# Optimization experiments

Hardware: AMD Instinct MI355X
Metric: run time of the kernel (lower is better)

## Reference

```python
import jax, jax.numpy as jnp
import numpy as np

# Model dims
L, B, S, D, H, V = 8, 4, 1024, 1024, 16, 256
FF = 4 * D
LN_EPS = 1e-5


def _ln(x, g, b):
    mu = jnp.mean(x, axis=-1, keepdims=True)
    var = jnp.mean(jnp.square(x - mu), axis=-1, keepdims=True)
    return (x - mu) * jax.lax.rsqrt(var + LN_EPS) * g + b


def setup_inputs() -> dict:
    key = jax.random.key(0)
    ks = jax.random.split(key, 12)
    p = lambda k, shape: (jax.random.normal(k, shape, jnp.float32) * 0.02)
    return {
        "input_tokens": jax.random.randint(ks[0], (B, S), 0, V),
        "tok_emb": p(ks[1], (V, D)),
        "pos_emb": p(ks[2], (S, D)),
        "Wq": p(ks[3], (L, D, D)),
        "Wk": p(ks[4], (L, D, D)),
        "Wv": p(ks[5], (L, D, D)),
        "Wo": p(ks[6], (L, D, D)),
        "bo": jnp.zeros((L, D), jnp.float32),
        "ln1_g": jnp.ones((L, D), jnp.float32),
        "ln1_b": jnp.zeros((L, D), jnp.float32),
        "ln2_g": jnp.ones((L, D), jnp.float32),
        "ln2_b": jnp.zeros((L, D), jnp.float32),
        "W1": p(ks[7], (L, D, FF)),
        "b1": jnp.zeros((L, FF), jnp.float32),
        "W2": p(ks[8], (L, FF, D)),
        "b2": jnp.zeros((L, D), jnp.float32),
        "lnf_g": jnp.ones((D,), jnp.float32),
        "lnf_b": jnp.zeros((D,), jnp.float32),
        "Wout": p(ks[9], (D, V)),
        "bout": jnp.zeros((V,), jnp.float32),
        "nhead": 16,
    }


def reference(input_tokens, tok_emb, pos_emb, Wq, Wk, Wv, Wo, bo,
              ln1_g, ln1_b, ln2_g, ln2_b, W1, b1, W2, b2,
              lnf_g, lnf_b, Wout, bout, nhead):
    b, s = input_tokens.shape
    d = tok_emb.shape[-1]
    hd = d // nhead
    scale = jnp.asarray(hd, jnp.float32) ** -0.5  # head_size ** -0.5
    mask = jnp.tril(jnp.ones((s, s), bool))  # causal

    x = tok_emb[input_tokens] + pos_emb[:s][None]  # [b,s,d]

    def block(x, p):
        wq, wk, wv, wo, bo_, g1, be1, g2, be2, w1, bf1, w2, bf2 = p
        h = _ln(x, g1, be1)
        q = (h @ wq).reshape(b, s, nhead, hd)
        k = (h @ wk).reshape(b, s, nhead, hd)
        v = (h @ wv).reshape(b, s, nhead, hd)
        scores = jnp.einsum('bqhd,bkhd->bhqk', q, k) * scale
        scores = jnp.where(mask, scores, -jnp.inf)
        attn = jax.nn.softmax(scores, axis=-1)  # dropout is identity (p=0 / eval)
        o = jnp.einsum('bhqk,bkhd->bqhd', attn, v).reshape(b, s, d)
        x = x + o @ wo + bo_
        h2 = _ln(x, g2, be2)
        x = x + jax.nn.relu(h2 @ w1 + bf1) @ w2 + bf2
        return x, None

    x, _ = jax.lax.scan(block, x, (Wq, Wk, Wv, Wo, bo, ln1_g, ln1_b,
                                   ln2_g, ln2_b, W1, b1, W2, b2))
    logits = _ln(x, lnf_g, lnf_b) @ Wout + bout  # [b,s,V]
    return logits
```

## Files before the change

kernel.cpp:

```cpp
#include <hip/hip_runtime.h>

#define DEV __device__ __forceinline__

typedef __bf16 bf16x8 __attribute__((ext_vector_type(8)));
typedef float  f32x4  __attribute__((ext_vector_type(4)));

typedef const __attribute__((address_space(1))) unsigned int* gas_ptr;
typedef       __attribute__((address_space(3))) unsigned int* las_ptr;

DEV unsigned short f2bf(float f) {
  union { __bf16 h; unsigned short u; } c; c.h = (__bf16)f; return c.u;
}

DEV float bf2f(unsigned short u) {
  union { unsigned int i; float f; } c; c.i = (unsigned int)u << 16; return c.f;
}

DEV void gll16(const void* g, void* l) {
  __builtin_amdgcn_global_load_lds((gas_ptr)g, (las_ptr)l, 16, 0, 0);
}

DEV f32x4 mfma16(bf16x8 a, bf16x8 b, f32x4 c) {
  return __builtin_amdgcn_mfma_f32_16x16x32_bf16(a, b, c, 0, 0, 0);
}

__global__ __launch_bounds__(256)
void tcvt_k(const float* __restrict__ src, unsigned short* __restrict__ dst,
            int K, int N)
{
  __shared__ float t[32][33];
  const int tx = threadIdx.x, ty = threadIdx.y;
  const size_t mo = (size_t)blockIdx.z * K * N;
  const int n0 = blockIdx.x * 32, k0 = blockIdx.y * 32;
  const float* s = src + mo;
  unsigned short* d = dst + mo;
#pragma unroll
  for (int i = 0; i < 4; i++)
    t[ty + i*8][tx] = s[(size_t)(k0 + ty + i*8) * N + n0 + tx];
  __syncthreads();
#pragma unroll
  for (int i = 0; i < 4; i++)
    d[(size_t)(n0 + ty + i*8) * K + k0 + tx] = f2bf(t[tx][ty + i*8]);
}

DEV void ln_tail(float4 s, const float* __restrict__ g,
                 const float* __restrict__ bta,
                 unsigned short* __restrict__ hrow, int t, float* red)
{
  float sm  = s.x + s.y + s.z + s.w;
  float sq = s.x*s.x + s.y*s.y + s.z*s.z + s.w*s.w;
#pragma unroll
  for (int mk = 32; mk >= 1; mk >>= 1) {
    sm += __shfl_xor(sm, mk);
    sq += __shfl_xor(sq, mk);
  }
  const int wv = t >> 6;
  if ((t & 63) == 0) { red[wv] = sm; red[4 + wv] = sq; }
  __syncthreads();
  sm = red[0] + red[1] + red[2] + red[3];
  sq = red[4] + red[5] + red[6] + red[7];
  const float mu = sm * (1.f/1024.f);
  const float rs = rsqrtf(sq * (1.f/1024.f) - mu*mu + 1e-5f);
  const float4 gv = ((const float4*)g)[t];
  const float4 bv = ((const float4*)bta)[t];
  ushort4 o;
  o.x = f2bf((s.x - mu) * rs * gv.x + bv.x);
  o.y = f2bf((s.y - mu) * rs * gv.y + bv.y);
  o.z = f2bf((s.z - mu) * rs * gv.z + bv.z);
  o.w = f2bf((s.w - mu) * rs * gv.w + bv.w);
  ((ushort4*)hrow)[t] = o;
}

__global__ __launch_bounds__(256)
void embed_ln_k(const int* __restrict__ toks, const float* __restrict__ te,
                const float* __restrict__ pe, const float* __restrict__ g,
                const float* __restrict__ bta,
                float* __restrict__ x, unsigned short* __restrict__ h)
{
  __shared__ float red[8];
  const int row = blockIdx.x, t = threadIdx.x;
  const int tok = toks[row], s = row & 1023;
  float4 a = ((const float4*)(te + (size_t)tok * 1024))[t];
  float4 p = ((const float4*)(pe + (size_t)s   * 1024))[t];
  float4 v; v.x = a.x+p.x; v.y = a.y+p.y; v.z = a.z+p.z; v.w = a.w+p.w;
  ((float4*)(x + (size_t)row * 1024))[t] = v;
  ln_tail(v, g, bta, h + (size_t)row * 1024, t, red);
}

__global__ __launch_bounds__(256)
void redln_k(const unsigned short* __restrict__ part,
             const float* __restrict__ bias,
             const float* __restrict__ g, const float* __restrict__ bta,
             float* __restrict__ x, unsigned short* __restrict__ h)
{
  __shared__ float red[8];
  const int row = blockIdx.x, t = threadIdx.x;
  const size_t pbase = (size_t)row * 1024 + t * 4;
  float a0 = 0.f, a1 = 0.f, a2 = 0.f, a3 = 0.f;
#pragma unroll
  for (int kz = 0; kz < 4; kz++) {
    ushort4 u = *(const ushort4*)&part[(size_t)kz * 4194304 + pbase];
    a0 += bf2f(u.x); a1 += bf2f(u.y); a2 += bf2f(u.z); a3 += bf2f(u.w);
  }
  float4 xv = ((const float4*)(x + (size_t)row * 1024))[t];
  float4 bv = ((const float4*)bias)[t];
  float4 s;
  s.x = xv.x + a0 + bv.x; s.y = xv.y + a1 + bv.y;
  s.z = xv.z + a2 + bv.z; s.w = xv.w + a3 + bv.w;
  ((float4*)(x + (size_t)row * 1024))[t] = s;
  ln_tail(s, g, bta, h + (size_t)row * 1024, t, red);
}

template<int EPI>
__global__ __launch_bounds__(256)
void gemm_k(const unsigned short* __restrict__ A,
            const unsigned short* __restrict__ B0,
            const unsigned short* __restrict__ B1,
            const unsigned short* __restrict__ B2,
            const float* __restrict__ bias,
            float* __restrict__ xio,
            unsigned short* __restrict__ o0,
            unsigned short* __restrict__ o1,
            unsigned short* __restrict__ o2,
            int K, int N, int Kc, float* __restrict__ part)
{
  __shared__ __align__(16) unsigned short As[2][128 * 32];
  __shared__ __align__(16) unsigned short Bs[2][128 * 32];
  const int tid = threadIdx.x;
  const int wave = tid >> 6, lane = tid & 63;
  const int wm = wave >> 1, wn = wave & 1;
  const int m0 = blockIdx.x * 128, n0 = blockIdx.y * 128;
  const int r16 = lane & 15, r4 = lane >> 4;

  const unsigned short* Bt = B0;
  if (EPI == 0) Bt = (blockIdx.z == 0) ? B0 : (blockIdx.z == 1) ? B1 : B2;
  const int koff = (EPI >= 4) ? blockIdx.z * Kc : 0;
  const int klen = (EPI >= 4) ? Kc : K;

  const unsigned short* ga = A  + (size_t)(m0 + (tid >> 2)) * K + koff + (tid & 3) * 8;
  const unsigned short* gb = Bt + (size_t)(n0 + (tid >> 2)) * K + koff + (tid & 3) * 8;
  const size_t rstep = (size_t)64 * K;
  const int lo = wave * 512;

  auto STAGE = [&](int slot, int tt) {
    const unsigned short* gaa = ga + tt * 32;
    const unsigned short* gbb = gb + tt * 32;
    gll16(gaa,         &As[slot][lo]);
    gll16(gaa + rstep, &As[slot][lo + 2048]);
    gll16(gbb,         &Bs[slot][lo]);
    gll16(gbb + rstep, &Bs[slot][lo + 2048]);
  };

  f32x4 acc[4][4] = {};
  const int NT = klen >> 5;

  STAGE(0, 0);
  if (NT > 1) STAGE(1, 1);

  for (int t = 0; t < NT; t++) {
    if (t + 1 < NT) asm volatile("s_waitcnt vmcnt(4)" ::: "memory");
    else            asm volatile("s_waitcnt vmcnt(0)" ::: "memory");
    __builtin_amdgcn_sched_barrier(0);
    __builtin_amdgcn_s_barrier();
    __builtin_amdgcn_sched_barrier(0);

    const int slot = t & 1;
    bf16x8 av[4], bv[4];
#pragma unroll
    for (int mf = 0; mf < 4; mf++)
      av[mf] = *(const bf16x8*)&As[slot][(wm*64 + mf*16 + r16) * 32 + r4 * 8];
#pragma unroll
    for (int nf = 0; nf < 4; nf++)
      bv[nf] = *(const bf16x8*)&Bs[slot][(wn*64 + nf*16 + r16) * 32 + r4 * 8];
    asm volatile("s_waitcnt lgkmcnt(0)" ::: "memory");
    __builtin_amdgcn_sched_barrier(0);
    __builtin_amdgcn_s_barrier();
    __builtin_amdgcn_sched_barrier(0);

    if (t + 2 < NT) STAGE(slot, t + 2);

#pragma unroll
    for (int mf = 0; mf < 4; mf++)
#pragma unroll
      for (int nf = 0; nf < 4; nf++)
        acc[mf][nf] = mfma16(av[mf], bv[nf], acc[mf][nf]);
    __builtin_amdgcn_sched_barrier(0);
  }

  const int row0 = m0 + wm * 64, col0 = n0 + wn * 64;
  float* po = nullptr;
  if (EPI == 4)
    po = part + (size_t)blockIdx.z * ((size_t)gridDim.x * 128 * N);
  unsigned short* po16 = nullptr;
  if (EPI == 5)
    po16 = o0 + (size_t)blockIdx.z * 4194304;
#pragma unroll
  for (int mf = 0; mf < 4; mf++) {
#pragma unroll
    for (int nf = 0; nf < 4; nf++) {
#pragma unroll
      for (int jj = 0; jj < 4; jj++) {
        const int r = row0 + mf*16 + r4*4 + jj;
        const int c = col0 + nf*16 + r16;
        const float v = acc[mf][nf][jj];
        if (EPI == 0) {
          const int z = blockIdx.z;
          const int b_ = r >> 10, s_ = r & 1023;
          const int hh = c >> 6, e = c & 63;
          if (z == 0)
            o0[((size_t)(b_*16 + hh) * 1024 + s_) * 64 + e] = f2bf(v * 0.125f);
          else if (z == 1)
            o1[((size_t)(b_*16 + hh) * 1024 + s_) * 64 + e] = f2bf(v);
          else
            o2[((size_t)(b_*16 + hh) * 64 + e) * 1024 + s_] = f2bf(v);
        } else if (EPI == 2) {
          const float t2 = v + bias[c];
          o0[(size_t)r * N + c] = f2bf(t2 > 0.f ? t2 : 0.f);
        } else if (EPI == 4) {
          po[(size_t)r * N + c] = v;
        } else if (EPI == 5) {
          po16[(size_t)r * N + c] = f2bf(v);
        }
      }
    }
  }
}

template<int EPI>
__global__ __launch_bounds__(512, 2)
void gemm8_k(const unsigned short* __restrict__ A,
             const unsigned short* __restrict__ Bt,
             const float* __restrict__ bias,
             unsigned short* __restrict__ o0,
             int K, int N, int Kc)
{
  __shared__ __align__(16) unsigned short LA[2][2][8192];
  __shared__ __align__(16) unsigned short LB[2][2][8192];
  const int tid = threadIdx.x;
  const int wave = tid >> 6, lane = tid & 63;
  const int wm = wave >> 2, wn = wave & 3;
  const int r16 = lane & 15, r4 = lane >> 4;
  const int m0 = blockIdx.x * 256, n0 = blockIdx.y * 256;
  const int koff = blockIdx.z * Kc;
  const int NT = Kc >> 6;

  const unsigned short* As0 = A  + (size_t)m0 * K + koff;
  const unsigned short* As1 = A  + (size_t)(m0 + 128) * K + koff;
  const unsigned short* Bs0 = Bt + (size_t)n0 * K + koff;
  const unsigned short* Bs1 = Bt + (size_t)(n0 + 128) * K + koff;

  auto STAGEH = [&](unsigned short* lds, const unsigned short* gsrc) {
    const int c0 = tid, r0 = c0 >> 3;
    gll16(gsrc + (size_t)r0 * K + ((c0 & 7) ^ (r0 & 7)) * 8, lds + c0 * 8);
    const int c1 = 512 + tid, r1 = c1 >> 3;
    gll16(gsrc + (size_t)r1 * K + ((c1 & 7) ^ (r1 & 7)) * 8, lds + c1 * 8);
  };

  f32x4 acc[8][4] = {};
  bf16x8 avx[4][2], bvx[2][2][2];

  STAGEH(&LB[0][0][0], Bs0);
  STAGEH(&LB[0][1][0], Bs1);
  STAGEH(&LA[0][0][0], As0);
  STAGEH(&LA[0][1][0], As1);
  if (NT > 1) {
    STAGEH(&LB[1][0][0], Bs0 + 64);
    STAGEH(&LB[1][1][0], Bs1 + 64);
  }

  for (int t = 0; t < NT; ++t) {
    const int slot = t & 1;
    if (t + 1 < NT) asm volatile("s_waitcnt vmcnt(4)" ::: "memory");
    else            asm volatile("s_waitcnt vmcnt(0)" ::: "memory");
    __builtin_amdgcn_sched_barrier(0);
    __builtin_amdgcn_s_barrier();
    __builtin_amdgcn_sched_barrier(0);

#pragma unroll
    for (int mfq = 0; mfq < 4; mfq++)
#pragma unroll
      for (int kk = 0; kk < 2; kk++)
        avx[mfq][kk] = *(const bf16x8*)&LA[slot][wm][
            (mfq*16 + r16) * 64 + (((kk*4 + r4) ^ (r16 & 7)) * 8)];
#pragma unroll
    for (int nfq = 0; nfq < 2; nfq++)
#pragma unroll
      for (int kk = 0; kk < 2; kk++)
        bvx[0][nfq][kk] = *(const bf16x8*)&LB[slot][wn >> 1][
            ((wn & 1)*64 + nfq*16 + r16) * 64 + (((kk*4 + r4) ^ (r16 & 7)) * 8)];
    if (t + 1 < NT) STAGEH(&LA[slot ^ 1][0][0], As0 + (t + 1) * 64);
    asm volatile("s_waitcnt lgkmcnt(0)" ::: "memory");
    __builtin_amdgcn_sched_barrier(0);
    __builtin_amdgcn_s_setprio(1);
#pragma unroll
    for (int mfq = 0; mfq < 4; mfq++)
#pragma unroll
      for (int nfq = 0; nfq < 2; nfq++)
#pragma unroll
        for (int kk = 0; kk < 2; kk++)
          acc[mfq][nfq] = mfma16(avx[mfq][kk], bvx[0][nfq][kk], acc[mfq][nfq]);
    __builtin_amdgcn_s_setprio(0);

#pragma unroll
    for (int nfq = 0; nfq < 2; nfq++)
#pragma unroll
      for (int kk = 0; kk < 2; kk++)
        bvx[1][nfq][kk] = *(const bf16x8*)&LB[slot][wn >> 1][
            ((wn & 1)*64 + 32 + nfq*16 + r16) * 64 + (((kk*4 + r4) ^ (r16 & 7)) * 8)];
    if (t + 1 < NT) STAGEH(&LA[slot ^ 1][1][0], As1 + (t + 1) * 64);
    asm volatile("s_waitcnt lgkmcnt(0)" ::: "memory");
    __builtin_amdgcn_sched_barrier(0);
    __builtin_amdgcn_s_setprio(1);
#pragma unroll
    for (int mfq = 0; mfq < 4; mfq++)
#pragma unroll
      for (int nfq = 0; nfq < 2; nfq++)
#pragma unroll
        for (int kk = 0; kk < 2; kk++)
          acc[mfq][2 + nfq] = mfma16(avx[mfq][kk], bvx[1][nfq][kk], acc[mfq][2 + nfq]);
    __builtin_amdgcn_s_setprio(0);

    __builtin_amdgcn_sched_barrier(0);
    __builtin_amdgcn_s_barrier();
    __builtin_amdgcn_sched_barrier(0);

#pragma unroll
    for (int mfq = 0; mfq < 4; mfq++)
#pragma unroll
      for (int kk = 0; kk < 2; kk++)
        avx[mfq][kk] = *(const bf16x8*)&LA[slot][wm][
            (64 + mfq*16 + r16) * 64 + (((kk*4 + r4) ^ (r16 & 7)) * 8)];
    if (t + 2 < NT) STAGEH(&LB[slot][0][0], Bs0 + (t + 2) * 64);
    asm volatile("s_waitcnt lgkmcnt(0)" ::: "memory");
    __builtin_amdgcn_sched_barrier(0);
    __builtin_amdgcn_s_setprio(1);
#pragma unroll
    for (int mfq = 0; mfq < 4; mfq++)
#pragma unroll
      for (int nfq = 0; nfq < 2; nfq++)
#pragma unroll
        for (int kk = 0; kk < 2; kk++)
          acc[4 + mfq][nfq] = mfma16(avx[mfq][kk], bvx[0][nfq][kk], acc[4 + mfq][nfq]);
    __builtin_amdgcn_s_setprio(0);

    if (t + 2 < NT) STAGEH(&LB[slot][1][0], Bs1 + (t + 2) * 64);
    __builtin_amdgcn_s_setprio(1);
#pragma unroll
    for (int mfq = 0; mfq < 4; mfq++)
#pragma unroll
      for (int nfq = 0; nfq < 2; nfq++)
#pragma unroll
        for (int kk = 0; kk < 2; kk++)
          acc[4 + mfq][2 + nfq] = mfma16(avx[mfq][kk], bvx[1][nfq][kk], acc[4 + mfq][2 + nfq]);
    __builtin_amdgcn_s_setprio(0);
    __builtin_amdgcn_sched_barrier(0);
  }

  const int row0 = m0 + wm * 128, col0 = n0 + wn * 64;
  unsigned short* po16 = o0;
  if (EPI == 5) po16 = o0 + (size_t)blockIdx.z * 4194304;
#pragma unroll
  for (int mf = 0; mf < 8; mf++) {
#pragma unroll
    for (int nf = 0; nf < 4; nf++) {
#pragma unroll
      for (int jj = 0; jj < 4; jj++) {
        const int r = row0 + mf*16 + r4*4 + jj;
        const int c = col0 + nf*16 + r16;
        const float v = acc[mf][nf][jj];
        if (EPI == 2) {
          const float t2 = v + bias[c];
          po16[(size_t)r * N + c] = f2bf(t2 > 0.f ? t2 : 0.f);
        } else {
          po16[(size_t)r * N + c] = f2bf(v);
        }
      }
    }
  }
}

__global__ __launch_bounds__(256)
void red_k(const float* __restrict__ part, const float* __restrict__ bias,
           float* __restrict__ outw, int n4, int nm4, int KZ)
{
  const float4* p4 = (const float4*)part;
  const float4* b4 = (const float4*)bias;
  for (size_t i = (size_t)blockIdx.x * 256 + threadIdx.x; i < (size_t)n4;
       i += (size_t)gridDim.x * 256) {
    float4 s = p4[i];
    for (int kz = 1; kz < KZ; kz++) {
      float4 t = p4[i + (size_t)kz * n4];
      s.x += t.x; s.y += t.y; s.z += t.z; s.w += t.w;
    }
    float4 bv = b4[i & nm4];
    s.x += bv.x; s.y += bv.y; s.z += bv.z; s.w += bv.w;
    ((float4*)outw)[i] = s;
  }
}

__global__ __launch_bounds__(256)
void attn_k(const unsigned short* __restrict__ qb,
            const unsigned short* __restrict__ kb,
            const unsigned short* __restrict__ vtb,
            unsigned short* __restrict__ att)
{
  __shared__ __align__(16) unsigned short Ks[2][64 * 64];
  __shared__ __align__(16) unsigned short Vs[2][64 * 64];
  __shared__ __align__(16) unsigned short Ps[64 * 72];
  const int flat = blockIdx.x;
  const int job  = (flat & 7) * 128 + (flat >> 3);
  const int qt   = 15 - (job & 15);
  const int h    = (job >> 4) & 15;
  const int b    = job >> 8;
  const int tid = threadIdx.x, wave = tid >> 6, lane = tid & 63;
  const int r16 = lane & 15, r4 = lane >> 4;
  const int q0 = qt * 64;
  const size_t bh = (size_t)(b * 16 + h);
  const unsigned short* qbh = qb  + bh * 1024 * 64;
  const unsigned short* kbh = kb  + bh * 1024 * 64;
  const unsigned short* vbh = vtb + bh * 64 * 1024;

  const int swz = ((lane & 7) ^ (lane >> 3)) * 8;
  const int srow = lane >> 3;

  auto STAGE = [&](int slot, int tt) {
    const int kv0 = tt * 64;
#pragma unroll
    for (int cc = 0; cc < 2; cc++) {
      const int chunk = wave * 2 + cc;
      gll16(kbh + (size_t)(kv0 + chunk*8 + srow) * 64 + swz,   &Ks[slot][chunk * 512]);
      gll16(vbh + (size_t)(chunk*8 + srow) * 1024 + kv0 + swz, &Vs[slot][chunk * 512]);
    }
  };

  bf16x8 qf[2];
#pragma unroll
  for (int kc = 0; kc < 2; kc++)
    qf[kc] = *(const bf16x8*)&qbh[(size_t)(q0 + wave*16 + r16) * 64 + kc*32 + r4*8];

  f32x4 oacc[4] = {};
  float l_i[4] = {0.f, 0.f, 0.f, 0.f};

  const int nt = qt + 1;

  STAGE(0, 0);
  if (nt > 1) STAGE(1, 1);

  for (int t = 0; t < nt; t++) {
    if (t + 1 < nt) asm volatile("s_waitcnt vmcnt(4)" ::: "memory");
    else            asm volatile("s_waitcnt vmcnt(0)" ::: "memory");
    __builtin_amdgcn_sched_barrier(0);
    __builtin_amdgcn_s_barrier();
    __builtin_amdgcn_sched_barrier(0);

    const int slot = t & 1;
    bf16x8 kf[2][4], vf[2][4];
#pragma unroll
    for (int kc = 0; kc < 2; kc++)
#pragma unroll
      for (int nf = 0; nf < 4; nf++) {
        kf[kc][nf] = *(const bf16x8*)&Ks[slot][(nf*16 + r16) * 64 +
                                              (((kc*4 + r4) ^ (r16 & 7)) * 8)];
        vf[kc][nf] = *(const bf16x8*)&Vs[slot][(nf*16 + r16) * 64 +
                                              (((kc*4 + r4) ^ (r16 & 7)) * 8)];
      }
    asm volatile("s_waitcnt lgkmcnt(0)" ::: "memory");
    __builtin_amdgcn_sched_barrier(0);
    __builtin_amdgcn_s_barrier();
    __builtin_amdgcn_sched_barrier(0);

    if (t + 2 < nt) STAGE(slot, t + 2);

    f32x4 sacc[4] = {};
#pragma unroll
    for (int kc = 0; kc < 2; kc++)
#pragma unroll
      for (int nf = 0; nf < 4; nf++)
        sacc[nf] = mfma16(qf[kc], kf[kc][nf], sacc[nf]);

    const bool diag = (t == nt - 1);
#pragma unroll
    for (int jj = 0; jj < 4; jj++) {
      float vv[4];
#pragma unroll
      for (int nf = 0; nf < 4; nf++) vv[nf] = sacc[nf][jj];
      if (diag) {
        const int qrow_l = wave*16 + r4*4 + jj;
#pragma unroll
        for (int nf = 0; nf < 4; nf++)
          if (nf*16 + r16 > qrow_l) vv[nf] = -1e30f;
      }
      float p0 = __expf(vv[0]), p1 = __expf(vv[1]);
      float p2 = __expf(vv[2]), p3 = __expf(vv[3]);
      l_i[jj] += (p0 + p1) + (p2 + p3);
      const int prow = (wave*16 + r4*4 + jj) * 72;
      Ps[prow + r16     ] = f2bf(p0);
      Ps[prow + 16 + r16] = f2bf(p1);
      Ps[prow + 32 + r16] = f2bf(p2);
      Ps[prow + 48 + r16] = f2bf(p3);
    }

#pragma unroll
    for (int kc = 0; kc < 2; kc++) {
      bf16x8 pf = *(const bf16x8*)&Ps[(wave*16 + r16) * 72 + kc*32 + r4*8];
#pragma unroll
      for (int nh = 0; nh < 4; nh++)
        oacc[nh] = mfma16(pf, vf[kc][nh], oacc[nh]);
    }
    __builtin_amdgcn_sched_barrier(0);
  }

#pragma unroll
  for (int jj = 0; jj < 4; jj++)
#pragma unroll
    for (int mk = 8; mk >= 1; mk >>= 1) l_i[jj] += __shfl_xor(l_i[jj], mk);

#pragma unroll
  for (int nh = 0; nh < 4; nh++) {
#pragma unroll
    for (int jj = 0; jj < 4; jj++) {
      const int row = q0 + wave*16 + r4*4 + jj;
      const int col = nh*16 + r16;
      const float o = oacc[nh][jj] / l_i[jj];
      att[(size_t)(b * 1024 + row) * 1024 + h*64 + col] = f2bf(o);
    }
  }
}

extern "C" void kernel_launch(void* const* d_in, const int* in_sizes, int n_in,
                              void* d_out, int out_size, void* d_ws, size_t ws_size,
                              hipStream_t stream)
{
  const int*   toks    = (const int*)  d_in[0];
  const float* tok_emb = (const float*)d_in[1];
  const float* pos_emb = (const float*)d_in[2];
  const float* Wq      = (const float*)d_in[3];
  const float* Wk      = (const float*)d_in[4];
  const float* Wv      = (const float*)d_in[5];
  const float* Wo      = (const float*)d_in[6];
  const float* bo      = (const float*)d_in[7];
  const float* ln1_g   = (const float*)d_in[8];
  const float* ln1_b   = (const float*)d_in[9];
  const float* ln2_g   = (const float*)d_in[10];
  const float* ln2_b   = (const float*)d_in[11];
  const float* W1      = (const float*)d_in[12];
  const float* b1      = (const float*)d_in[13];
  const float* W2      = (const float*)d_in[14];
  const float* b2      = (const float*)d_in[15];
  const float* lnf_g   = (const float*)d_in[16];
  const float* lnf_b   = (const float*)d_in[17];
  const float* Wout    = (const float*)d_in[18];
  const float* bout    = (const float*)d_in[19];
  float* out = (float*)d_out;

  char* w = (char*)d_ws;
  size_t off = 0;
  auto alloc = [&](size_t bytes) -> void* {
    void* p = w + off; off += (bytes + 255) & ~(size_t)255; return p;
  };
  unsigned short* wqT   = (unsigned short*)alloc(8ull*1024*1024*2);
  unsigned short* wkT   = (unsigned short*)alloc(8ull*1024*1024*2);
  unsigned short* wvT   = (unsigned short*)alloc(8ull*1024*1024*2);
  unsigned short* woT   = (unsigned short*)alloc(8ull*1024*1024*2);
  unsigned short* w1T   = (unsigned short*)alloc(8ull*1024*4096*2);
  unsigned short* w2T   = (unsigned short*)alloc(8ull*4096*1024*2);
  unsigned short* woutT = (unsigned short*)alloc(256ull*1024*2);
  float*          x     = (float*)         alloc(4096ull*1024*4);
  unsigned short* hbuf  = (unsigned short*)alloc(4096ull*1024*2);
  unsigned short* qbuf  = (unsigned short*)alloc(64ull*1024*64*2);
  unsigned short* kbuf  = (unsigned short*)alloc(64ull*1024*64*2);
  unsigned short* vtb   = (unsigned short*)alloc(64ull*1024*64*2);
  unsigned short* att   = (unsigned short*)alloc(4096ull*1024*2);
  unsigned short* ff    = (unsigned short*)alloc(4096ull*4096*2);
  unsigned short* part16= (unsigned short*)alloc(4ull*4194304*2);
  float*          part  = (float*)         alloc(8ull*1048576*4);
  (void)ws_size; (void)in_sizes; (void)n_in; (void)out_size;

  dim3 tb(32, 8);
  tcvt_k<<<dim3(32, 32, 8),  tb, 0, stream>>>(Wq,   wqT,   1024, 1024);
  tcvt_k<<<dim3(32, 32, 8),  tb, 0, stream>>>(Wk,   wkT,   1024, 1024);
  tcvt_k<<<dim3(32, 32, 8),  tb, 0, stream>>>(Wv,   wvT,   1024, 1024);
  tcvt_k<<<dim3(32, 32, 8),  tb, 0, stream>>>(Wo,   woT,   1024, 1024);
  tcvt_k<<<dim3(128, 32, 8), tb, 0, stream>>>(W1,   w1T,   1024, 4096);
  tcvt_k<<<dim3(32, 128, 8), tb, 0, stream>>>(W2,   w2T,   4096, 1024);
  tcvt_k<<<dim3(8, 32, 1),   tb, 0, stream>>>(Wout, woutT, 1024, 256);

  embed_ln_k<<<4096, 256, 0, stream>>>(toks, tok_emb, pos_emb,
                                       ln1_g, ln1_b, x, hbuf);

  for (int l = 0; l < 8; l++) {
    gemm_k<0><<<dim3(32, 8, 3), 256, 0, stream>>>(hbuf,
        wqT + (size_t)l*1048576, wkT + (size_t)l*1048576, wvT + (size_t)l*1048576,
        nullptr, nullptr, qbuf, kbuf, vtb, 1024, 1024, 1024, nullptr);
    attn_k<<<1024, 256, 0, stream>>>(qbuf, kbuf, vtb, att);
    gemm_k<5><<<dim3(32, 8, 4), 256, 0, stream>>>(att,
        woT + (size_t)l*1048576, nullptr, nullptr,
        nullptr, nullptr, part16, nullptr, nullptr, 1024, 1024, 256, nullptr);
    redln_k<<<4096, 256, 0, stream>>>(part16, bo + l*1024,
        ln2_g + l*1024, ln2_b + l*1024, x, hbuf);
    gemm8_k<2><<<dim3(16, 16), 512, 0, stream>>>(hbuf,
        w1T + (size_t)l*4194304, b1 + l*4096, ff, 1024, 4096, 1024);
    gemm8_k<5><<<dim3(16, 4, 4), 512, 0, stream>>>(ff,
        w2T + (size_t)l*4194304, nullptr, part16, 4096, 1024, 1024);
    if (l < 7)
      redln_k<<<4096, 256, 0, stream>>>(part16, b2 + l*1024,
          ln1_g + (l+1)*1024, ln1_b + (l+1)*1024, x, hbuf);
    else
      redln_k<<<4096, 256, 0, stream>>>(part16, b2 + l*1024,
          lnf_g, lnf_b, x, hbuf);
  }

  gemm_k<4><<<dim3(32, 2, 8), 256, 0, stream>>>(hbuf, woutT, nullptr, nullptr,
      nullptr, nullptr, nullptr, nullptr, nullptr, 1024, 256, 128, part);
  red_k<<<1024, 256, 0, stream>>>(part, bout, out, 262144, 63, 8);
}
```

Measured before the change: 1.707 ms.

## Move QKV and out-proj GEMMs to 256x256 tile kernel; enlarge attention q-tile

The QKV projection and attention output projection now use the 512-thread 256x256-tile GEMM kernel (with the QKV scatter epilogue moved into it) instead of the 128x128 kernel. gemm_k is reduced to the split-K fp32 path used only for the final logits. The attention kernel now processes 128 query rows per 512-thread block, sharing each K/V tile across 8 waves, and skips waves whose rows are fully masked. The aim is more data reuse per block and fewer blocks per launch, at the cost of fewer blocks for the QKV GEMM (192) and idle waves in causal tiles.

```diff
diff --git a/kernel.cpp b/kernel.cpp
--- a/kernel.cpp
+++ b/kernel.cpp
@@ -115,13 +115,6 @@
 __global__ __launch_bounds__(256)
 void gemm_k(const unsigned short* __restrict__ A,
             const unsigned short* __restrict__ B0,
-            const unsigned short* __restrict__ B1,
-            const unsigned short* __restrict__ B2,
-            const float* __restrict__ bias,
-            float* __restrict__ xio,
-            unsigned short* __restrict__ o0,
-            unsigned short* __restrict__ o1,
-            unsigned short* __restrict__ o2,
             int K, int N, int Kc, float* __restrict__ part)
 {
   __shared__ __align__(16) unsigned short As[2][128 * 32];
@@ -132,13 +125,10 @@
   const int m0 = blockIdx.x * 128, n0 = blockIdx.y * 128;
   const int r16 = lane & 15, r4 = lane >> 4;
 
-  const unsigned short* Bt = B0;
-  if (EPI == 0) Bt = (blockIdx.z == 0) ? B0 : (blockIdx.z == 1) ? B1 : B2;
-  const int koff = (EPI >= 4) ? blockIdx.z * Kc : 0;
-  const int klen = (EPI >= 4) ? Kc : K;
+  const int koff = blockIdx.z * Kc;
 
   const unsigned short* ga = A  + (size_t)(m0 + (tid >> 2)) * K + koff + (tid & 3) * 8;
-  const unsigned short* gb = Bt + (size_t)(n0 + (tid >> 2)) * K + koff + (tid & 3) * 8;
+  const unsigned short* gb = B0 + (size_t)(n0 + (tid >> 2)) * K + koff + (tid & 3) * 8;
   const size_t rstep = (size_t)64 * K;
   const int lo = wave * 512;
 
@@ -152,7 +142,7 @@
   };
 
   f32x4 acc[4][4] = {};
-  const int NT = klen >> 5;
+  const int NT = Kc >> 5;
 
   STAGE(0, 0);
   if (NT > 1) STAGE(1, 1);
@@ -188,14 +178,161 @@
   }
 
   const int row0 = m0 + wm * 64, col0 = n0 + wn * 64;
-  float* po = nullptr;
-  if (EPI == 4)
-    po = part + (size_t)blockIdx.z * ((size_t)gridDim.x * 128 * N);
-  unsigned short* po16 = nullptr;
-  if (EPI == 5)
-    po16 = o0 + (size_t)blockIdx.z * 4194304;
-#pragma unroll
-  for (int mf = 0; mf < 4; mf++) {
+  float* po = part + (size_t)blockIdx.z * ((size_t)gridDim.x * 128 * N);
+#pragma unroll
+  for (int mf = 0; mf < 4; mf++)
+#pragma unroll
+    for (int nf = 0; nf < 4; nf++)
+#pragma unroll
+      for (int jj = 0; jj < 4; jj++) {
+        const int r = row0 + mf*16 + r4*4 + jj;
+        const int c = col0 + nf*16 + r16;
+        po[(size_t)r * N + c] = acc[mf][nf][jj];
+      }
+}
+
+template<int EPI>
+__global__ __launch_bounds__(512, 2)
+void gemm8_k(const unsigned short* __restrict__ A,
+             const unsigned short* __restrict__ B0,
+             const unsigned short* __restrict__ B1,
+             const unsigned short* __restrict__ B2,
+             const float* __restrict__ bias,
+             unsigned short* __restrict__ o0,
+             unsigned short* __restrict__ o1,
+             unsigned short* __restrict__ o2,
+             int K, int N, int Kc)
+{
+  __shared__ __align__(16) unsigned short LA[2][2][8192];
+  __shared__ __align__(16) unsigned short LB[2][2][8192];
+  const int tid = threadIdx.x;
+  const int wave = tid >> 6, lane = tid & 63;
+  const int wm = wave >> 2, wn = wave & 3;
+  const int r16 = lane & 15, r4 = lane >> 4;
+  const int m0 = blockIdx.x * 256, n0 = blockIdx.y * 256;
+  const int koff = (EPI == 5) ? blockIdx.z * Kc : 0;
+  const int NT = Kc >> 6;
+
+  const unsigned short* Bt = B0;
+  if (EPI == 0) Bt = (blockIdx.z == 0) ? B0 : (blockIdx.z == 1) ? B1 : B2;
+
+  const unsigned short* As0 = A  + (size_t)m0 * K + koff;
+  const unsigned short* As1 = A  + (size_t)(m0 + 128) * K + koff;
+  const unsigned short* Bs0 = Bt + (size_t)n0 * K + koff;
+  const unsigned short* Bs1 = Bt + (size_t)(n0 + 128) * K + koff;
+
+  auto STAGEH = [&](unsigned short* lds, const unsigned short* gsrc) {
+    const int c0 = tid, r0 = c0 >> 3;
+    gll16(gsrc + (size_t)r0 * K + ((c0 & 7) ^ (r0 & 7)) * 8, lds + c0 * 8);
+    const int c1 = 512 + tid, r1 = c1 >> 3;
+    gll16(gsrc + (size_t)r1 * K + ((c1 & 7) ^ (r1 & 7)) * 8, lds + c1 * 8);
+  };
+
+  f32x4 acc[8][4] = {};
+  bf16x8 avx[4][2], bvx[2][2][2];
+
+  STAGEH(&LB[0][0][0], Bs0);
+  STAGEH(&LB[0][1][0], Bs1);
+  STAGEH(&LA[0][0][0], As0);
+  STAGEH(&LA[0][1][0], As1);
+  if (NT > 1) {
+    STAGEH(&LB[1][0][0], Bs0 + 64);
+    STAGEH(&LB[1][1][0], Bs1 + 64);
+  }
+
+  for (int t = 0; t < NT; ++t) {
+    const int slot = t & 1;
+    if (t + 1 < NT) asm volatile("s_waitcnt vmcnt(4)" ::: "memory");
+    else            asm volatile("s_waitcnt vmcnt(0)" ::: "memory");
+    __builtin_amdgcn_sched_barrier(0);
+    __builtin_amdgcn_s_barrier();
+    __builtin_amdgcn_sched_barrier(0);
+
+#pragma unroll
+    for (int mfq = 0; mfq < 4; mfq++)
+#pragma unroll
+      for (int kk = 0; kk < 2; kk++)
+        avx[mfq][kk] = *(const bf16x8*)&LA[slot][wm][
+            (mfq*16 + r16) * 64 + (((kk*4 + r4) ^ (r16 & 7)) * 8)];
+#pragma unroll
+    for (int nfq = 0; nfq < 2; nfq++)
+#pragma unroll
+      for (int kk = 0; kk < 2; kk++)
+        bvx[0][nfq][kk] = *(const bf16x8*)&LB[slot][wn >> 1][
+            ((wn & 1)*64 + nfq*16 + r16) * 64 + (((kk*4 + r4) ^ (r16 & 7)) * 8)];
+    if (t + 1 < NT) STAGEH(&LA[slot ^ 1][0][0], As0 + (t + 1) * 64);
+    asm volatile("s_waitcnt lgkmcnt(0)" ::: "memory");
+    __builtin_amdgcn_sched_barrier(0);
+    __builtin_amdgcn_s_setprio(1);
+#pragma unroll
+    for (int mfq = 0; mfq < 4; mfq++)
+#pragma unroll
+      for (int nfq = 0; nfq < 2; nfq++)
+#pragma unroll
+        for (int kk = 0; kk < 2; kk++)
+          acc[mfq][nfq] = mfma16(avx[mfq][kk], bvx[0][nfq][kk], acc[mfq][nfq]);
+    __builtin_amdgcn_s_setprio(0);
+
+#pragma unroll
+    for (int nfq = 0; nfq < 2; nfq++)
+#pragma unroll
+      for (int kk = 0; kk < 2; kk++)
+        bvx[1][nfq][kk] = *(const bf16x8*)&LB[slot][wn >> 1][
+            ((wn & 1)*64 + 32 + nfq*16 + r16) * 64 + (((kk*4 + r4) ^ (r16 & 7)) * 8)];
+    if (t + 1 < NT) STAGEH(&LA[slot ^ 1][1][0], As1 + (t + 1) * 64);
+    asm volatile("s_waitcnt lgkmcnt(0)" ::: "memory");
+    __builtin_amdgcn_sched_barrier(0);
+    __builtin_amdgcn_s_setprio(1);
+#pragma unroll
+    for (int mfq = 0; mfq < 4; mfq++)
+#pragma unroll
+      for (int nfq = 0; nfq < 2; nfq++)
+#pragma unroll
+        for (int kk = 0; kk < 2; kk++)
+          acc[mfq][2 + nfq] = mfma16(avx[mfq][kk], bvx[1][nfq][kk], acc[mfq][2 + nfq]);
+    __builtin_amdgcn_s_setprio(0);
+
+    __builtin_amdgcn_sched_barrier(0);
+    __builtin_amdgcn_s_barrier();
+    __builtin_amdgcn_sched_barrier(0);
+
+#pragma unroll
+    for (int mfq = 0; mfq < 4; mfq++)
+#pragma unroll
+      for (int kk = 0; kk < 2; kk++)
+        avx[mfq][kk] = *(const bf16x8*)&LA[slot][wm][
+            (64 + mfq*16 + r16) * 64 + (((kk*4 + r4) ^ (r16 & 7)) * 8)];
+    if (t + 2 < NT) STAGEH(&LB[slot][0][0], Bs0 + (t + 2) * 64);
+    asm volatile("s_waitcnt lgkmcnt(0)" ::: "memory");
+    __builtin_amdgcn_sched_barrier(0);
+    __builtin_amdgcn_s_setprio(1);
+#pragma unroll
+    for (int mfq = 0; mfq < 4; mfq++)
+#pragma unroll
+      for (int nfq = 0; nfq < 2; nfq++)
+#pragma unroll
+        for (int kk = 0; kk < 2; kk++)
+          acc[4 + mfq][nfq] = mfma16(avx[mfq][kk], bvx[0][nfq][kk], acc[4 + mfq][nfq]);
+    __builtin_amdgcn_s_setprio(0);
+
+    if (t + 2 < NT) STAGEH(&LB[slot][1][0], Bs1 + (t + 2) * 64);
+    __builtin_amdgcn_s_setprio(1);
+#pragma unroll
+    for (int mfq = 0; mfq < 4; mfq++)
+#pragma unroll
+      for (int nfq = 0; nfq < 2; nfq++)
+#pragma unroll
+        for (int kk = 0; kk < 2; kk++)
+          acc[4 + mfq][2 + nfq] = mfma16(avx[mfq][kk], bvx[1][nfq][kk], acc[4 + mfq][2 + nfq]);
+    __builtin_amdgcn_s_setprio(0);
+    __builtin_amdgcn_sched_barrier(0);
+  }
+
+  const int row0 = m0 + wm * 128, col0 = n0 + wn * 64;
+  unsigned short* po16 = o0;
+  if (EPI == 5) po16 = o0 + (size_t)blockIdx.z * 4194304;
+#pragma unroll
+  for (int mf = 0; mf < 8; mf++) {
 #pragma unroll
     for (int nf = 0; nf < 4; nf++) {
 #pragma unroll
@@ -215,161 +352,6 @@
             o2[((size_t)(b_*16 + hh) * 64 + e) * 1024 + s_] = f2bf(v);
         } else if (EPI == 2) {
           const float t2 = v + bias[c];
-          o0[(size_t)r * N + c] = f2bf(t2 > 0.f ? t2 : 0.f);
-        } else if (EPI == 4) {
-          po[(size_t)r * N + c] = v;
-        } else if (EPI == 5) {
-          po16[(size_t)r * N + c] = f2bf(v);
-        }
-      }
-    }
-  }
-}
-
-template<int EPI>
-__global__ __launch_bounds__(512, 2)
-void gemm8_k(const unsigned short* __restrict__ A,
-             const unsigned short* __restrict__ Bt,
-             const float* __restrict__ bias,
-             unsigned short* __restrict__ o0,
-             int K, int N, int Kc)
-{
-  __shared__ __align__(16) unsigned short LA[2][2][8192];
-  __shared__ __align__(16) unsigned short LB[2][2][8192];
-  const int tid = threadIdx.x;
-  const int wave = tid >> 6, lane = tid & 63;
-  const int wm = wave >> 2, wn = wave & 3;
-  const int r16 = lane & 15, r4 = lane >> 4;
-  const int m0 = blockIdx.x * 256, n0 = blockIdx.y * 256;
-  const int koff = blockIdx.z * Kc;
-  const int NT = Kc >> 6;
-
-  const unsigned short* As0 = A  + (size_t)m0 * K + koff;
-  const unsigned short* As1 = A  + (size_t)(m0 + 128) * K + koff;
-  const unsigned short* Bs0 = Bt + (size_t)n0 * K + koff;
-  const unsigned short* Bs1 = Bt + (size_t)(n0 + 128) * K + koff;
-
-  auto STAGEH = [&](unsigned short* lds, const unsigned short* gsrc) {
-    const int c0 = tid, r0 = c0 >> 3;
-    gll16(gsrc + (size_t)r0 * K + ((c0 & 7) ^ (r0 & 7)) * 8, lds + c0 * 8);
-    const int c1 = 512 + tid, r1 = c1 >> 3;
-    gll16(gsrc + (size_t)r1 * K + ((c1 & 7) ^ (r1 & 7)) * 8, lds + c1 * 8);
-  };
-
-  f32x4 acc[8][4] = {};
-  bf16x8 avx[4][2], bvx[2][2][2];
-
-  STAGEH(&LB[0][0][0], Bs0);
-  STAGEH(&LB[0][1][0], Bs1);
-  STAGEH(&LA[0][0][0], As0);
-  STAGEH(&LA[0][1][0], As1);
-  if (NT > 1) {
-    STAGEH(&LB[1][0][0], Bs0 + 64);
-    STAGEH(&LB[1][1][0], Bs1 + 64);
-  }
-
-  for (int t = 0; t < NT; ++t) {
-    const int slot = t & 1;
-    if (t + 1 < NT) asm volatile("s_waitcnt vmcnt(4)" ::: "memory");
-    else            asm volatile("s_waitcnt vmcnt(0)" ::: "memory");
-    __builtin_amdgcn_sched_barrier(0);
-    __builtin_amdgcn_s_barrier();
-    __builtin_amdgcn_sched_barrier(0);
-
-#pragma unroll
-    for (int mfq = 0; mfq < 4; mfq++)
-#pragma unroll
-      for (int kk = 0; kk < 2; kk++)
-        avx[mfq][kk] = *(const bf16x8*)&LA[slot][wm][
-            (mfq*16 + r16) * 64 + (((kk*4 + r4) ^ (r16 & 7)) * 8)];
-#pragma unroll
-    for (int nfq = 0; nfq < 2; nfq++)
-#pragma unroll
-      for (int kk = 0; kk < 2; kk++)
-        bvx[0][nfq][kk] = *(const bf16x8*)&LB[slot][wn >> 1][
-            ((wn & 1)*64 + nfq*16 + r16) * 64 + (((kk*4 + r4) ^ (r16 & 7)) * 8)];
-    if (t + 1 < NT) STAGEH(&LA[slot ^ 1][0][0], As0 + (t + 1) * 64);
-    asm volatile("s_waitcnt lgkmcnt(0)" ::: "memory");
-    __builtin_amdgcn_sched_barrier(0);
-    __builtin_amdgcn_s_setprio(1);
-#pragma unroll
-    for (int mfq = 0; mfq < 4; mfq++)
-#pragma unroll
-      for (int nfq = 0; nfq < 2; nfq++)
-#pragma unroll
-        for (int kk = 0; kk < 2; kk++)
-          acc[mfq][nfq] = mfma16(avx[mfq][kk], bvx[0][nfq][kk], acc[mfq][nfq]);
-    __builtin_amdgcn_s_setprio(0);
-
-#pragma unroll
-    for (int nfq = 0; nfq < 2; nfq++)
-#pragma unroll
-      for (int kk = 0; kk < 2; kk++)
-        bvx[1][nfq][kk] = *(const bf16x8*)&LB[slot][wn >> 1][
-            ((wn & 1)*64 + 32 + nfq*16 + r16) * 64 + (((kk*4 + r4) ^ (r16 & 7)) * 8)];
-    if (t + 1 < NT) STAGEH(&LA[slot ^ 1][1][0], As1 + (t + 1) * 64);
-    asm volatile("s_waitcnt lgkmcnt(0)" ::: "memory");
-    __builtin_amdgcn_sched_barrier(0);
-    __builtin_amdgcn_s_setprio(1);
-#pragma unroll
-    for (int mfq = 0; mfq < 4; mfq++)
-#pragma unroll
-      for (int nfq = 0; nfq < 2; nfq++)
-#pragma unroll
-        for (int kk = 0; kk < 2; kk++)
-          acc[mfq][2 + nfq] = mfma16(avx[mfq][kk], bvx[1][nfq][kk], acc[mfq][2 + nfq]);
-    __builtin_amdgcn_s_setprio(0);
-
-    __builtin_amdgcn_sched_barrier(0);
-    __builtin_amdgcn_s_barrier();
-    __builtin_amdgcn_sched_barrier(0);
-
-#pragma unroll
-    for (int mfq = 0; mfq < 4; mfq++)
-#pragma unroll
-      for (int kk = 0; kk < 2; kk++)
-        avx[mfq][kk] = *(const bf16x8*)&LA[slot][wm][
-            (64 + mfq*16 + r16) * 64 + (((kk*4 + r4) ^ (r16 & 7)) * 8)];
-    if (t + 2 < NT) STAGEH(&LB[slot][0][0], Bs0 + (t + 2) * 64);
-    asm volatile("s_waitcnt lgkmcnt(0)" ::: "memory");
-    __builtin_amdgcn_sched_barrier(0);
-    __builtin_amdgcn_s_setprio(1);
-#pragma unroll
-    for (int mfq = 0; mfq < 4; mfq++)
-#pragma unroll
-      for (int nfq = 0; nfq < 2; nfq++)
-#pragma unroll
-        for (int kk = 0; kk < 2; kk++)
-          acc[4 + mfq][nfq] = mfma16(avx[mfq][kk], bvx[0][nfq][kk], acc[4 + mfq][nfq]);
-    __builtin_amdgcn_s_setprio(0);
-
-    if (t + 2 < NT) STAGEH(&LB[slot][1][0], Bs1 + (t + 2) * 64);
-    __builtin_amdgcn_s_setprio(1);
-#pragma unroll
-    for (int mfq = 0; mfq < 4; mfq++)
-#pragma unroll
-      for (int nfq = 0; nfq < 2; nfq++)
-#pragma unroll
-        for (int kk = 0; kk < 2; kk++)
-          acc[4 + mfq][2 + nfq] = mfma16(avx[mfq][kk], bvx[1][nfq][kk], acc[4 + mfq][2 + nfq]);
-    __builtin_amdgcn_s_setprio(0);
-    __builtin_amdgcn_sched_barrier(0);
-  }
-
-  const int row0 = m0 + wm * 128, col0 = n0 + wn * 64;
-  unsigned short* po16 = o0;
-  if (EPI == 5) po16 = o0 + (size_t)blockIdx.z * 4194304;
-#pragma unroll
-  for (int mf = 0; mf < 8; mf++) {
-#pragma unroll
-    for (int nf = 0; nf < 4; nf++) {
-#pragma unroll
-      for (int jj = 0; jj < 4; jj++) {
-        const int r = row0 + mf*16 + r4*4 + jj;
-        const int c = col0 + nf*16 + r16;
-        const float v = acc[mf][nf][jj];
-        if (EPI == 2) {
-          const float t2 = v + bias[c];
           po16[(size_t)r * N + c] = f2bf(t2 > 0.f ? t2 : 0.f);
         } else {
           po16[(size_t)r * N + c] = f2bf(v);
@@ -398,7 +380,7 @@
   }
 }
 
-__global__ __launch_bounds__(256)
+__global__ __launch_bounds__(512)
 void attn_k(const unsigned short* __restrict__ qb,
             const unsigned short* __restrict__ kb,
             const unsigned short* __restrict__ vtb,
@@ -406,120 +388,123 @@
 {
   __shared__ __align__(16) unsigned short Ks[2][64 * 64];
   __shared__ __align__(16) unsigned short Vs[2][64 * 64];
-  __shared__ __align__(16) unsigned short Ps[64 * 72];
+  __shared__ __align__(16) unsigned short Ps[128 * 72];
   const int flat = blockIdx.x;
-  const int job  = (flat & 7) * 128 + (flat >> 3);
-  const int qt   = 15 - (job & 15);
-  const int h    = (job >> 4) & 15;
-  const int b    = job >> 8;
+  const int job  = (flat & 7) * 64 + (flat >> 3);
+  const int qt   = 7 - (job & 7);
+  const int h    = (job >> 3) & 15;
+  const int b    = job >> 7;
   const int tid = threadIdx.x, wave = tid >> 6, lane = tid & 63;
   const int r16 = lane & 15, r4 = lane >> 4;
-  const int q0 = qt * 64;
+  const int q0 = qt * 128;
   const size_t bh = (size_t)(b * 16 + h);
   const unsigned short* qbh = qb  + bh * 1024 * 64;
   const unsigned short* kbh = kb  + bh * 1024 * 64;
   const unsigned short* vbh = vtb + bh * 64 * 1024;
 
-  const int swz = ((lane & 7) ^ (lane >> 3)) * 8;
-  const int srow = lane >> 3;
-
+  const int srow = tid >> 3;
+  const int swz  = ((tid & 7) ^ (srow & 7)) * 8;
   auto STAGE = [&](int slot, int tt) {
     const int kv0 = tt * 64;
-#pragma unroll
-    for (int cc = 0; cc < 2; cc++) {
-      const int chunk = wave * 2 + cc;
-      gll16(kbh + (size_t)(kv0 + chunk*8 + srow) * 64 + swz,   &Ks[slot][chunk * 512]);
-      gll16(vbh + (size_t)(chunk*8 + srow) * 1024 + kv0 + swz, &Vs[slot][chunk * 512]);
-    }
+    gll16(kbh + (size_t)(kv0 + srow) * 64 + swz,   &Ks[slot][tid * 8]);
+    gll16(vbh + (size_t)srow * 1024 + kv0 + swz,   &Vs[slot][tid * 8]);
   };
 
+  const int wrow0 = q0 + wave * 16;
   bf16x8 qf[2];
 #pragma unroll
   for (int kc = 0; kc < 2; kc++)
-    qf[kc] = *(const bf16x8*)&qbh[(size_t)(q0 + wave*16 + r16) * 64 + kc*32 + r4*8];
+    qf[kc] = *(const bf16x8*)&qbh[(size_t)(wrow0 + r16) * 64 + kc*32 + r4*8];
 
   f32x4 oacc[4] = {};
   float l_i[4] = {0.f, 0.f, 0.f, 0.f};
 
-  const int nt = qt + 1;
+  const int nt = 2 * qt + 2;
 
   STAGE(0, 0);
   if (nt > 1) STAGE(1, 1);
 
   for (int t = 0; t < nt; t++) {
-    if (t + 1 < nt) asm volatile("s_waitcnt vmcnt(4)" ::: "memory");
+    if (t + 1 < nt) asm volatile("s_waitcnt vmcnt(2)" ::: "memory");
     else            asm volatile("s_waitcnt vmcnt(0)" ::: "memory");
     __builtin_amdgcn_sched_barrier(0);
     __builtin_amdgcn_s_barrier();
     __builtin_amdgcn_sched_barrier(0);
 
     const int slot = t & 1;
+    const int kv0 = t * 64;
+    const bool active = (kv0 <= wrow0 + 15);
+
     bf16x8 kf[2][4], vf[2][4];
-#pragma unroll
-    for (int kc = 0; kc < 2; kc++)
-#pragma unroll
-      for (int nf = 0; nf < 4; nf++) {
-        kf[kc][nf] = *(const bf16x8*)&Ks[slot][(nf*16 + r16) * 64 +
-                                              (((kc*4 + r4) ^ (r16 & 7)) * 8)];
-        vf[kc][nf] = *(const bf16x8*)&Vs[slot][(nf*16 + r16) * 64 +
-                                              (((kc*4 + r4) ^ (r16 & 7)) * 8)];
+    if (active) {
+#pragma unroll
+      for (int kc = 0; kc < 2; kc++)
+#pragma unroll
+        for (int nf = 0; nf < 4; nf++) {
+          kf[kc][nf] = *(const bf16x8*)&Ks[slot][(nf*16 + r16) * 64 +
+                                                (((kc*4 + r4) ^ (r16 & 7)) * 8)];
+          vf[kc][nf] = *(const bf16x8*)&Vs[slot][(nf*16 + r16) * 64 +
+                                                (((kc*4 + r4) ^ (r16 & 7)) * 8)];
+        }
+    }
+    asm volatile("s_waitcnt lgkmcnt(0)" ::: "memory");
+    __builtin_amdgcn_sched_barrier(0);
+    __builtin_amdgcn_s_barrier();
+    __builtin_amdgcn_sched_barrier(0);
+
+    if (t + 2 < nt) STAGE(slot, t + 2);
+
+    if (active) {
+      f32x4 sacc[4] = {};
+#pragma unroll
+      for (int kc = 0; kc < 2; kc++)
+#pragma unroll
+        for (int nf = 0; nf < 4; nf++)
+          sacc[nf] = mfma16(qf[kc], kf[kc][nf], sacc[nf]);
+
+      const bool needmask = (kv0 + 63 > wrow0);
+#pragma unroll
+      for (int jj = 0; jj < 4; jj++) {
+        float vv[4];
+#pragma unroll
+        for (int nf = 0; nf < 4; nf++) vv[nf] = sacc[nf][jj];
+        if (needmask) {
+          const int qrow = wrow0 + r4*4 + jj;
+#pragma unroll
+          for (int nf = 0; nf < 4; nf++)
+            if (kv0 + nf*16 + r16 > qrow) vv[nf] = -1e30f;
+        }
+        float p0 = __expf(vv[0]), p1 = __expf(vv[1]);
+        float p2 = __expf(vv[2]), p3 = __expf(vv[3]);
+        l_i[jj] += (p0 + p1) + (p2 + p3);
+        const int prow = (wave*16 + r4*4 + jj) * 72;
+        Ps[prow + r16     ] = f2bf(p0);
+        Ps[prow + 16 + r16] = f2bf(p1);
+        Ps[prow + 32 + r16] = f2bf(p2);
+        Ps[prow + 48 + r16] = f2bf(p3);
       }
-    asm volatile("s_waitcnt lgkmcnt(0)" ::: "memory");
-    __builtin_amdgcn_sched_barrier(0);
-    __builtin_amdgcn_s_barrier();
-    __builtin_amdgcn_sched_barrier(0);
-
-    if (t + 2 < nt) STAGE(slot, t + 2);
-
-    f32x4 sacc[4] = {};
-#pragma unroll
-    for (int kc = 0; kc < 2; kc++)
-#pragma unroll
-      for (int nf = 0; nf < 4; nf++)
-        sacc[nf] = mfma16(qf[kc], kf[kc][nf], sacc[nf]);
-
-    const bool diag = (t == nt - 1);
+
+#pragma unroll
+      for (int kc = 0; kc < 2; kc++) {
+        bf16x8 pf = *(const bf16x8*)&Ps[(wave*16 + r16) * 72 + kc*32 + r4*8];
+#pragma unroll
+        for (int nh = 0; nh < 4; nh++)
+          oacc[nh] = mfma16(pf, vf[kc][nh], oacc[nh]);
+      }
+    }
+    __builtin_amdgcn_sched_barrier(0);
+  }
+
+#pragma unroll
+  for (int jj = 0; jj < 4; jj++)
+#pragma unroll
+    for (int mk = 8; mk >= 1; mk >>= 1) l_i[jj] += __shfl_xor(l_i[jj], mk);
+
+#pragma unroll
+  for (int nh = 0; nh < 4; nh++) {
 #pragma unroll
     for (int jj = 0; jj < 4; jj++) {
-      float vv[4];
-#pragma unroll
-      for (int nf = 0; nf < 4; nf++) vv[nf] = sacc[nf][jj];
-      if (diag) {
-        const int qrow_l = wave*16 + r4*4 + jj;
-#pragma unroll
-        for (int nf = 0; nf < 4; nf++)
-          if (nf*16 + r16 > qrow_l) vv[nf] = -1e30f;
-      }
-      float p0 = __expf(vv[0]), p1 = __expf(vv[1]);
-      float p2 = __expf(vv[2]), p3 = __expf(vv[3]);
-      l_i[jj] += (p0 + p1) + (p2 + p3);
-      const int prow = (wave*16 + r4*4 + jj) * 72;
-      Ps[prow + r16     ] = f2bf(p0);
-      Ps[prow + 16 + r16] = f2bf(p1);
-      Ps[prow + 32 + r16] = f2bf(p2);
-      Ps[prow + 48 + r16] = f2bf(p3);
-    }
-
-#pragma unroll
-    for (int kc = 0; kc < 2; kc++) {
-      bf16x8 pf = *(const bf16x8*)&Ps[(wave*16 + r16) * 72 + kc*32 + r4*8];
-#pragma unroll
-      for (int nh = 0; nh < 4; nh++)
-        oacc[nh] = mfma16(pf, vf[kc][nh], oacc[nh]);
-    }
-    __builtin_amdgcn_sched_barrier(0);
-  }
-
-#pragma unroll
-  for (int jj = 0; jj < 4; jj++)
-#pragma unroll
-    for (int mk = 8; mk >= 1; mk >>= 1) l_i[jj] += __shfl_xor(l_i[jj], mk);
-
-#pragma unroll
-  for (int nh = 0; nh < 4; nh++) {
-#pragma unroll
-    for (int jj = 0; jj < 4; jj++) {
-      const int row = q0 + wave*16 + r4*4 + jj;
+      const int row = wrow0 + r4*4 + jj;
       const int col = nh*16 + r16;
       const float o = oacc[nh][jj] / l_i[jj];
       att[(size_t)(b * 1024 + row) * 1024 + h*64 + col] = f2bf(o);
@@ -589,19 +574,21 @@
                                        ln1_g, ln1_b, x, hbuf);
 
   for (int l = 0; l < 8; l++) {
-    gemm_k<0><<<dim3(32, 8, 3), 256, 0, stream>>>(hbuf,
+    gemm8_k<0><<<dim3(16, 4, 3), 512, 0, stream>>>(hbuf,
         wqT + (size_t)l*1048576, wkT + (size_t)l*1048576, wvT + (size_t)l*1048576,
-        nullptr, nullptr, qbuf, kbuf, vtb, 1024, 1024, 1024, nullptr);
-    attn_k<<<1024, 256, 0, stream>>>(qbuf, kbuf, vtb, att);
-    gemm_k<5><<<dim3(32, 8, 4), 256, 0, stream>>>(att,
+        nullptr, qbuf, kbuf, vtb, 1024, 1024, 1024);
+    attn_k<<<512, 512, 0, stream>>>(qbuf, kbuf, vtb, att);
+    gemm8_k<5><<<dim3(16, 4, 4), 512, 0, stream>>>(att,
         woT + (size_t)l*1048576, nullptr, nullptr,
-        nullptr, nullptr, part16, nullptr, nullptr, 1024, 1024, 256, nullptr);
+        nullptr, part16, nullptr, nullptr, 1024, 1024, 256);
     redln_k<<<4096, 256, 0, stream>>>(part16, bo + l*1024,
         ln2_g + l*1024, ln2_b + l*1024, x, hbuf);
     gemm8_k<2><<<dim3(16, 16), 512, 0, stream>>>(hbuf,
-        w1T + (size_t)l*4194304, b1 + l*4096, ff, 1024, 4096, 1024);
+        w1T + (size_t)l*4194304, nullptr, nullptr,
+        b1 + l*4096, ff, nullptr, nullptr, 1024, 4096, 1024);
     gemm8_k<5><<<dim3(16, 4, 4), 512, 0, stream>>>(ff,
-        w2T + (size_t)l*4194304, nullptr, part16, 4096, 1024, 1024);
+        w2T + (size_t)l*4194304, nullptr, nullptr,
+        nullptr, part16, nullptr, nullptr, 4096, 1024, 1024);
     if (l < 7)
       redln_k<<<4096, 256, 0, stream>>>(part16, b2 + l*1024,
           ln1_g + (l+1)*1024, ln1_b + (l+1)*1024, x, hbuf);
@@ -610,7 +597,7 @@
           lnf_g, lnf_b, x, hbuf);
   }
 
-  gemm_k<4><<<dim3(32, 2, 8), 256, 0, stream>>>(hbuf, woutT, nullptr, nullptr,
-      nullptr, nullptr, nullptr, nullptr, nullptr, 1024, 256, 128, part);
+  gemm_k<4><<<dim3(32, 2, 8), 256, 0, stream>>>(hbuf, woutT,
+      1024, 256, 128, part);
   red_k<<<1024, 256, 0, stream>>>(part, bout, out, 262144, 63, 8);
 }
```

Result: slower. 1.847 ms (+8.2%).
